# Optimization experiments

Hardware: AMD Instinct MI355X
Metric: run time of the kernel (lower is better)

Reference implementation:

```python
import jax, jax.numpy as jnp
import numpy as np

EMBED_DIM = 256
N_LEVELS = 4
N_HEADS = 8
N_POINTS = 4
HEAD_DIM = EMBED_DIM // N_HEADS
N_QUERIES = 8192
BATCH = 2
LEVEL_SHAPES = np.array([[128, 128], [64, 64], [32, 32], [16, 16]], dtype=np.int32)
HMAX, WMAX = 128, 128
EPS = 1e-5


def setup_inputs() -> dict:
    key = jax.random.key(0)
    ks = jax.random.split(key, 10)
    scale = 1.0 / np.sqrt(EMBED_DIM)
    query = jax.random.normal(ks[0], (N_QUERIES, EMBED_DIM), jnp.float32)
    xy_reference_points = jax.random.uniform(ks[1], (N_QUERIES, 2), jnp.float32, 0.05, 0.95)
    val = jax.random.normal(ks[2], (BATCH, HMAX, WMAX, N_LEVELS, EMBED_DIM), jnp.float32)
    # zero outside each level's valid support (mimics sparse COO: absent entries read as 0)
    hh = jnp.arange(HMAX)[:, None, None]
    ww = jnp.arange(WMAX)[None, :, None]
    lh = jnp.asarray(LEVEL_SHAPES[:, 0])[None, None, :]
    lw = jnp.asarray(LEVEL_SHAPES[:, 1])[None, None, :]
    mask = ((hh < lh) & (ww < lw)).astype(jnp.float32)
    stacked_value_tensors = val * mask[None, :, :, :, None]
    return {
        "query": query,
        "xy_reference_points": xy_reference_points,
        "stacked_value_tensors": stacked_value_tensors,
        "W_off": (jax.random.normal(ks[3], (EMBED_DIM, N_LEVELS * N_POINTS * N_HEADS * 2)) * scale * 0.1).astype(jnp.float32),
        "b_off": (jax.random.normal(ks[4], (N_LEVELS * N_POINTS * N_HEADS * 2,)) * 0.5).astype(jnp.float32),
        "W_attn": (jax.random.normal(ks[5], (EMBED_DIM, N_LEVELS * N_POINTS * N_HEADS)) * scale).astype(jnp.float32),
        "b_attn": jnp.zeros((N_LEVELS * N_POINTS * N_HEADS,), jnp.float32),
        "W_out": (jax.random.normal(ks[6], (EMBED_DIM, EMBED_DIM)) * scale).astype(jnp.float32),
        "b_out": jnp.zeros((EMBED_DIM,), jnp.float32),
        "batch_offsets": jnp.array([0, N_QUERIES // 2], jnp.int32),
        "spatial_shapes": jnp.asarray(LEVEL_SHAPES, jnp.int32),
    }


def reference(query, xy_reference_points, stacked_value_tensors, W_off, b_off,
              W_attn, b_attn, W_out, b_out, batch_offsets, spatial_shapes):
    Q = query.shape[0]
    # sampling offsets & attention weights (torch Linear with W stored [in,out])
    off = (query @ W_off + b_off).reshape(Q, N_LEVELS, N_POINTS, N_HEADS, 2)
    aw = (query @ W_attn + b_attn).reshape(Q, N_LEVELS * N_POINTS, N_HEADS)
    aw = jax.nn.softmax(aw, axis=1).reshape(Q, N_LEVELS, N_POINTS, N_HEADS)
    # sampling locations: sigmoid(inverse_sigmoid(ref) + offsets), then map (0,1)->(-1,1)
    r = jnp.clip(xy_reference_points, 0.0, 1.0)
    inv = jnp.log(jnp.clip(r, EPS, 1.0) / jnp.clip(1.0 - r, EPS, 1.0))
    loc = jax.nn.sigmoid(inv[:, None, None, None, :] + off) * 2.0 - 1.0  # (Q,L,P,H,2)
    # per-query batch index from batch_offsets (start index per batch element)
    bidx = jnp.searchsorted(batch_offsets, jnp.arange(Q), side="right") - 1  # (Q,)
    b = bidx[:, None, None, None]
    h_sz = spatial_shapes[:, 0].astype(loc.dtype)[None, :, None, None]
    w_sz = spatial_shapes[:, 1].astype(loc.dtype)[None, :, None, None]
    x = ((loc[..., 0] + 1.0) * w_sz - 1.0) / 2.0  # (Q,L,P,H)
    y = ((loc[..., 1] + 1.0) * h_sz - 1.0) / 2.0
    x0 = jnp.floor(x).astype(jnp.int32); x1 = x0 + 1
    y0 = jnp.floor(y).astype(jnp.int32); y1 = y0 + 1
    wcap = (spatial_shapes[:, 1] - 1).astype(jnp.int32)[None, :, None, None]
    hcap = (spatial_shapes[:, 0] - 1).astype(jnp.int32)[None, :, None, None]
    x0 = jnp.clip(x0, 0, wcap); x1 = jnp.clip(x1, 0, wcap)
    y0 = jnp.clip(y0, 0, hcap); y1 = jnp.clip(y1, 0, hcap)
    x0f = x0.astype(x.dtype); x1f = x1.astype(x.dtype)
    y0f = y0.astype(y.dtype); y1f = y1.astype(y.dtype)
    wa = (x1f - x) * (y1f - y)  # pairs with (x0,y0), as in source
    wb = (x1f - x) * (y - y0f)  # (x0,y1)
    wc = (x - x0f) * (y1f - y)  # (x1,y0)
    wd = (x - x0f) * (y - y0f)  # (x1,y1)
    V = stacked_value_tensors.reshape(BATCH, HMAX, WMAX, N_LEVELS, N_HEADS, HEAD_DIM)
    l = jnp.arange(N_LEVELS)[None, :, None, None]
    h = jnp.arange(N_HEADS)[None, None, None, :]
    # NOTE: source indexes (batch, x, y, level, head) -> x indexes the height dim; levels are square
    def g(xi, yi):
        return V[b, xi, yi, l, h]  # (Q,L,P,H,HEAD_DIM)
    sampled = (wa[..., None] * g(x0, y0) + wb[..., None] * g(x0, y1)
               + wc[..., None] * g(x1, y0) + wd[..., None] * g(x1, y1))
    out = jnp.einsum("qlphd,qlph->qhd", sampled, aw).reshape(Q, EMBED_DIM)
    return out @ W_out + b_out
```

## Files before the change

kernel.cpp:

```cpp
#include <hip/hip_runtime.h>
#include <math.h>

#define ED      256
#define NL      4
#define NH      8
#define NP      4
#define HD      32
#define HMAX    128
#define WMAX    128
#define NLP     16
#define NC      128
#define NOFF_AW 384
#define QPB     4
#define BSTRIDE (HMAX*WMAX*NL*ED)
#define XSTRIDE (WMAX*NL*ED)
#define YSTRIDE (NL*ED)

typedef __attribute__((ext_vector_type(8))) short bf16x8;
typedef __attribute__((ext_vector_type(4))) float f32x4;

__device__ __forceinline__ unsigned short f2bf(float x) {
    unsigned int u = __float_as_uint(x);
    u = (u + 0x7fffu + ((u >> 16) & 1u)) >> 16;
    return (unsigned short)u;
}
__device__ __forceinline__ float bf2f(unsigned short h) {
    unsigned int u = ((unsigned int)h) << 16;
    return __uint_as_float(u);
}

__global__ __launch_bounds__(256) void msda_convert_kernel(
    const float* __restrict__ query,
    const float* __restrict__ W_off,
    const float* __restrict__ W_attn,
    const float* __restrict__ W_out,
    unsigned short* __restrict__ qh,
    unsigned short* __restrict__ ql,
    unsigned short* __restrict__ BTh,
    unsigned short* __restrict__ BTl,
    unsigned short* __restrict__ WoutT,
    int nq)
{
    const int idx = blockIdx.x * 256 + threadIdx.x;
    const int t1 = nq * ED;
    const int t2 = NOFF_AW * ED;
    const int t3 = ED * ED;
    if (idx < t1) {
        float v = query[idx];
        unsigned short h = f2bf(v);
        qh[idx] = h;
        ql[idx] = f2bf(v - bf2f(h));
    } else if (idx < t1 + t2) {
        int i = idx - t1;
        int c = i >> 8, e = i & 255;
        float v = (c < ED) ? W_off[e * ED + c] : W_attn[e * NC + (c - ED)];
        unsigned short h = f2bf(v);
        BTh[i] = h;
        BTl[i] = f2bf(v - bf2f(h));
    } else if (idx < t1 + t2 + t3) {
        int i = idx - t1 - t2;
        int c = i >> 8, e = i & 255;
        WoutT[i] = f2bf(W_out[e * ED + c]);
    }
}

__global__ __launch_bounds__(256) void gemm_split_kernel(
    const unsigned short* __restrict__ Ah,
    const unsigned short* __restrict__ Al,
    const unsigned short* __restrict__ BTh,
    const unsigned short* __restrict__ BTl,
    const float* __restrict__ bias0,
    const float* __restrict__ bias1,
    float* __restrict__ C,
    int M, int NTOT, int bias_split)
{
    const int wave = threadIdx.x >> 6;
    const int lane = threadIdx.x & 63;
    const int gw   = blockIdx.x * 4 + wave;
    const int ngroups = NTOT >> 6;
    const int mg = gw / ngroups, ng = gw % ngroups;
    const int m16 = mg * 16, n64 = ng * 64;
    if (m16 >= M) return;

    const int mrow = lane & 15;
    const int quad = lane >> 4;

    const bf16x8* Ahp = (const bf16x8*)(Ah + (size_t)(m16 + mrow) * 256 + quad * 8);
    const bf16x8* Alp = (const bf16x8*)(Al + (size_t)(m16 + mrow) * 256 + quad * 8);
    const bf16x8* Bh0 = (const bf16x8*)(BTh + (size_t)(n64 +  0 + mrow) * 256 + quad * 8);
    const bf16x8* Bh1 = (const bf16x8*)(BTh + (size_t)(n64 + 16 + mrow) * 256 + quad * 8);
    const bf16x8* Bh2 = (const bf16x8*)(BTh + (size_t)(n64 + 32 + mrow) * 256 + quad * 8);
    const bf16x8* Bh3 = (const bf16x8*)(BTh + (size_t)(n64 + 48 + mrow) * 256 + quad * 8);
    const bf16x8* Bl0 = (const bf16x8*)(BTl + (size_t)(n64 +  0 + mrow) * 256 + quad * 8);
    const bf16x8* Bl1 = (const bf16x8*)(BTl + (size_t)(n64 + 16 + mrow) * 256 + quad * 8);
    const bf16x8* Bl2 = (const bf16x8*)(BTl + (size_t)(n64 + 32 + mrow) * 256 + quad * 8);
    const bf16x8* Bl3 = (const bf16x8*)(BTl + (size_t)(n64 + 48 + mrow) * 256 + quad * 8);

    f32x4 acc0 = {0.f,0.f,0.f,0.f}, acc1 = acc0, acc2 = acc0, acc3 = acc0;
    #pragma unroll
    for (int kb = 0; kb < 8; ++kb) {
        bf16x8 ah = Ahp[kb * 4];
        bf16x8 al = Alp[kb * 4];
        bf16x8 b0 = Bh0[kb * 4], b1 = Bh1[kb * 4], b2 = Bh2[kb * 4], b3 = Bh3[kb * 4];
        acc0 = __builtin_amdgcn_mfma_f32_16x16x32_bf16(ah, b0, acc0, 0, 0, 0);
        acc1 = __builtin_amdgcn_mfma_f32_16x16x32_bf16(ah, b1, acc1, 0, 0, 0);
        acc2 = __builtin_amdgcn_mfma_f32_16x16x32_bf16(ah, b2, acc2, 0, 0, 0);
        acc3 = __builtin_amdgcn_mfma_f32_16x16x32_bf16(ah, b3, acc3, 0, 0, 0);
        acc0 = __builtin_amdgcn_mfma_f32_16x16x32_bf16(al, b0, acc0, 0, 0, 0);
        acc1 = __builtin_amdgcn_mfma_f32_16x16x32_bf16(al, b1, acc1, 0, 0, 0);
        acc2 = __builtin_amdgcn_mfma_f32_16x16x32_bf16(al, b2, acc2, 0, 0, 0);
        acc3 = __builtin_amdgcn_mfma_f32_16x16x32_bf16(al, b3, acc3, 0, 0, 0);
        acc0 = __builtin_amdgcn_mfma_f32_16x16x32_bf16(ah, Bl0[kb * 4], acc0, 0, 0, 0);
        acc1 = __builtin_amdgcn_mfma_f32_16x16x32_bf16(ah, Bl1[kb * 4], acc1, 0, 0, 0);
        acc2 = __builtin_amdgcn_mfma_f32_16x16x32_bf16(ah, Bl2[kb * 4], acc2, 0, 0, 0);
        acc3 = __builtin_amdgcn_mfma_f32_16x16x32_bf16(ah, Bl3[kb * 4], acc3, 0, 0, 0);
    }

    const int col = lane & 15;
    f32x4 accs[4] = {acc0, acc1, acc2, acc3};
    #pragma unroll
    for (int i = 0; i < 4; ++i) {
        int n = n64 + i * 16 + col;
        float b = (n < bias_split) ? bias0[n] : bias1[n - bias_split];
        #pragma unroll
        for (int r = 0; r < 4; ++r) {
            int row = m16 + quad * 4 + r;
            C[(size_t)row * NTOT + n] = accs[i][r] + b;
        }
    }
}

__global__ __launch_bounds__(256) void gemm_bf16_kernel(
    const unsigned short* __restrict__ A,
    const unsigned short* __restrict__ BT,
    const float* __restrict__ bias,
    float* __restrict__ C,
    int M, int NTOT)
{
    const int wave = threadIdx.x >> 6;
    const int lane = threadIdx.x & 63;
    const int gw   = blockIdx.x * 4 + wave;
    const int ngroups = NTOT >> 6;
    const int mg = gw / ngroups, ng = gw % ngroups;
    const int m16 = mg * 16, n64 = ng * 64;
    if (m16 >= M) return;

    const int mrow = lane & 15;
    const int quad = lane >> 4;

    const bf16x8* Arow = (const bf16x8*)(A + (size_t)(m16 + mrow) * 256 + quad * 8);
    const bf16x8* B0 = (const bf16x8*)(BT + (size_t)(n64 +  0 + mrow) * 256 + quad * 8);
    const bf16x8* B1 = (const bf16x8*)(BT + (size_t)(n64 + 16 + mrow) * 256 + quad * 8);
    const bf16x8* B2 = (const bf16x8*)(BT + (size_t)(n64 + 32 + mrow) * 256 + quad * 8);
    const bf16x8* B3 = (const bf16x8*)(BT + (size_t)(n64 + 48 + mrow) * 256 + quad * 8);

    f32x4 acc0 = {0.f,0.f,0.f,0.f}, acc1 = acc0, acc2 = acc0, acc3 = acc0;
    #pragma unroll
    for (int kb = 0; kb < 8; ++kb) {
        bf16x8 af = Arow[kb * 4];
        acc0 = __builtin_amdgcn_mfma_f32_16x16x32_bf16(af, B0[kb * 4], acc0, 0, 0, 0);
        acc1 = __builtin_amdgcn_mfma_f32_16x16x32_bf16(af, B1[kb * 4], acc1, 0, 0, 0);
        acc2 = __builtin_amdgcn_mfma_f32_16x16x32_bf16(af, B2[kb * 4], acc2, 0, 0, 0);
        acc3 = __builtin_amdgcn_mfma_f32_16x16x32_bf16(af, B3[kb * 4], acc3, 0, 0, 0);
    }

    const int col = lane & 15;
    f32x4 accs[4] = {acc0, acc1, acc2, acc3};
    #pragma unroll
    for (int i = 0; i < 4; ++i) {
        int n = n64 + i * 16 + col;
        float b = bias[n];
        #pragma unroll
        for (int r = 0; r < 4; ++r) {
            int row = m16 + quad * 4 + r;
            C[(size_t)row * NTOT + n] = accs[i][r] + b;
        }
    }
}

__global__ __launch_bounds__(256) void msda_sample_kernel(
    const float* __restrict__ refp,
    const float* __restrict__ V,
    const float* __restrict__ off_aw,
    const int*   __restrict__ batch_off,
    int n_batch,
    const int*   __restrict__ spatial,
    unsigned short* __restrict__ out_pre,
    int q_total)
{
    __shared__ float  law[QPB][NC];
    __shared__ float2 sminv[QPB][NH];
    __shared__ float2 sref[QPB];
    __shared__ int4   soff[QPB][NC];
    __shared__ float4 swt[QPB][NC];

    const int t  = threadIdx.x;
    const int q0 = blockIdx.x * QPB;

    {
        const int s = t >> 6, c = t & 63;
        const float* row = off_aw + (size_t)(q0 + s) * NOFF_AW + ED;
        law[s][c]      = row[c];
        law[s][c + 64] = row[c + 64];
    }
    __syncthreads();

    if (t < QPB * NH) {
        const int s = t >> 3, h = t & 7;
        float m = -1e30f;
        #pragma unroll
        for (int lp = 0; lp < NLP; ++lp) m = fmaxf(m, law[s][lp * NH + h]);
        float sum = 0.f;
        #pragma unroll
        for (int lp = 0; lp < NLP; ++lp) sum += __expf(law[s][lp * NH + h] - m);
        sminv[s][h] = make_float2(m, 1.f / sum);
    } else if (t < QPB * NH + QPB) {
        const int s = t - QPB * NH;
        const int qid = q0 + s;
        float rx = refp[qid * 2 + 0], ry = refp[qid * 2 + 1];
        rx = fminf(fmaxf(rx, 0.f), 1.f);
        ry = fminf(fmaxf(ry, 0.f), 1.f);
        float ivx = __logf(fmaxf(rx, 1e-5f) / fmaxf(1.f - rx, 1e-5f));
        float ivy = __logf(fmaxf(ry, 1e-5f) / fmaxf(1.f - ry, 1e-5f));
        sref[s] = make_float2(ivx, ivy);
    }
    __syncthreads();

    {
        const int s = t >> 6;
        const int qid = q0 + s;
        int b = 0;
        for (int i = 1; i < n_batch; ++i)
            if (batch_off[i] <= qid) b = i;
        const int bbase = b * BSTRIDE;
        const float2 iv = sref[s];
        const float* offrow = off_aw + (size_t)qid * NOFF_AW;

        #pragma unroll
        for (int half = 0; half < 2; ++half) {
            const int c = (t & 63) + half * 64;
            const int l = c >> 5;
            const int h = c & 7;
            const int hsz = spatial[l * 2 + 0];
            const int wsz = spatial[l * 2 + 1];
            const int wcap = wsz - 1, hcap = hsz - 1;

            const float2 mi = sminv[s][h];
            const float a = __expf(law[s][c] - mi.x) * mi.y;

            const float ox = offrow[c * 2 + 0], oy = offrow[c * 2 + 1];
            float lx = 2.f / (1.f + __expf(-(iv.x + ox))) - 1.f;
            float ly = 2.f / (1.f + __expf(-(iv.y + oy))) - 1.f;
            float x = ((lx + 1.f) * (float)wsz - 1.f) * 0.5f;
            float y = ((ly + 1.f) * (float)hsz - 1.f) * 0.5f;
            int x0 = (int)floorf(x), y0 = (int)floorf(y);
            int x1 = x0 + 1, y1 = y0 + 1;
            x0 = min(max(x0, 0), wcap); x1 = min(max(x1, 0), wcap);
            y0 = min(max(y0, 0), hcap); y1 = min(max(y1, 0), hcap);
            float x0f = (float)x0, x1f = (float)x1;
            float y0f = (float)y0, y1f = (float)y1;

            float4 w;
            w.x = a * (x1f - x) * (y1f - y);
            w.y = a * (x1f - x) * (y - y0f);
            w.z = a * (x - x0f) * (y1f - y);
            w.w = a * (x - x0f) * (y - y0f);
            swt[s][c] = w;
            const int lbase = bbase + l * ED;
            int4 o;
            o.x = lbase + x0 * XSTRIDE + y0 * YSTRIDE;
            o.y = lbase + x0 * XSTRIDE + y1 * YSTRIDE;
            o.z = lbase + x1 * XSTRIDE + y0 * YSTRIDE;
            o.w = lbase + x1 * XSTRIDE + y1 * YSTRIDE;
            soff[s][c] = o;
        }
    }
    __syncthreads();

    {
        const int s    = t >> 6;
        const int lane = t & 63;
        const int h    = lane >> 3;
        const int d4   = (lane & 7) << 2;
        const int inner = h * HD + d4;
        float4 acc = {0.f, 0.f, 0.f, 0.f};
        #pragma unroll 4
        for (int lp = 0; lp < NLP; ++lp) {
            const int c = lp * NH + h;
            int4   o = soff[s][c];
            float4 w = swt[s][c];
            float4 v0 = *(const float4*)&V[o.x + inner];
            float4 v1 = *(const float4*)&V[o.y + inner];
            float4 v2 = *(const float4*)&V[o.z + inner];
            float4 v3 = *(const float4*)&V[o.w + inner];
            acc.x += w.x*v0.x + w.y*v1.x + w.z*v2.x + w.w*v3.x;
            acc.y += w.x*v0.y + w.y*v1.y + w.z*v2.y + w.w*v3.y;
            acc.z += w.x*v0.z + w.y*v1.z + w.z*v2.z + w.w*v3.z;
            acc.w += w.x*v0.w + w.y*v1.w + w.z*v2.w + w.w*v3.w;
        }
        ushort4 o4;
        o4.x = f2bf(acc.x); o4.y = f2bf(acc.y);
        o4.z = f2bf(acc.z); o4.w = f2bf(acc.w);
        *(ushort4*)&out_pre[(size_t)(q0 + s) * ED + inner] = o4;
    }
}

extern "C" void kernel_launch(void* const* d_in, const int* in_sizes, int n_in,
                              void* d_out, int out_size, void* d_ws, size_t ws_size,
                              hipStream_t stream) {
    const float* query  = (const float*)d_in[0];
    const float* refp   = (const float*)d_in[1];
    const float* V      = (const float*)d_in[2];
    const float* W_off  = (const float*)d_in[3];
    const float* b_off  = (const float*)d_in[4];
    const float* W_attn = (const float*)d_in[5];
    const float* b_attn = (const float*)d_in[6];
    const float* W_out  = (const float*)d_in[7];
    const float* b_out  = (const float*)d_in[8];
    const int*   boff   = (const int*)d_in[9];
    const int*   spat   = (const int*)d_in[10];
    const int n_batch   = in_sizes[9];
    const int nq        = in_sizes[0] / ED;
    float* out = (float*)d_out;

    char* ws = (char*)d_ws;
    float*          off_aw  = (float*)ws;
    unsigned short* qh      = (unsigned short*)(ws + (size_t)nq*NOFF_AW*4);
    unsigned short* ql      = qh    + (size_t)nq*ED;
    unsigned short* BTh     = ql    + (size_t)nq*ED;
    unsigned short* BTl     = BTh   + NOFF_AW*ED;
    unsigned short* WoutT   = BTl   + NOFF_AW*ED;
    unsigned short* out_pre = WoutT + ED*ED;

    {
        int total = nq*ED + NOFF_AW*ED + ED*ED;
        msda_convert_kernel<<<(total + 255)/256, 256, 0, stream>>>(
            query, W_off, W_attn, W_out, qh, ql, BTh, BTl, WoutT, nq);
    }
    {
        int waves = (nq/16) * (NOFF_AW/64);
        gemm_split_kernel<<<(waves + 3)/4, 256, 0, stream>>>(
            qh, ql, BTh, BTl, b_off, b_attn, off_aw, nq, NOFF_AW, ED);
    }
    {
        msda_sample_kernel<<<nq/QPB, 256, 0, stream>>>(
            refp, V, off_aw, boff, n_batch, spat, out_pre, nq);
    }
    {
        int waves = (nq/16) * (ED/64);
        gemm_bf16_kernel<<<(waves + 3)/4, 256, 0, stream>>>(
            out_pre, WoutT, b_out, out, nq, ED);
    }
}
```

Before: 290.1 us.

## Switch offset GEMM to fp16 split-A with in-kernel query conversion

Replaces the bf16 hi/lo three-term split GEMM with an fp16 scheme: the weights are stored as a single fp16 copy and the fp32 query is split into fp16 hi/lo inside the GEMM kernel, so only two MFMA passes run per k-step. This removes the separate query conversion pass and its workspace writes and reads, and cuts MFMA count by a third. fp16's longer mantissa is meant to keep offset precision without the weight-low term, but it risks range and rounding differences in the computed offsets.

```diff
diff --git a/kernel.cpp b/kernel.cpp
--- a/kernel.cpp
+++ b/kernel.cpp
@@ -16,59 +16,40 @@
 #define XSTRIDE (WMAX*NL*ED)
 #define YSTRIDE (NL*ED)
 
-typedef __attribute__((ext_vector_type(8))) short bf16x8;
-typedef __attribute__((ext_vector_type(4))) float f32x4;
+typedef __attribute__((ext_vector_type(8))) short    bf16x8;
+typedef __attribute__((ext_vector_type(8))) __fp16   f16x8;
+typedef __attribute__((ext_vector_type(4))) float    f32x4;
 
 __device__ __forceinline__ unsigned short f2bf(float x) {
     unsigned int u = __float_as_uint(x);
     u = (u + 0x7fffu + ((u >> 16) & 1u)) >> 16;
     return (unsigned short)u;
 }
-__device__ __forceinline__ float bf2f(unsigned short h) {
-    unsigned int u = ((unsigned int)h) << 16;
-    return __uint_as_float(u);
-}
-
-__global__ __launch_bounds__(256) void msda_convert_kernel(
-    const float* __restrict__ query,
+
+__global__ __launch_bounds__(256) void msda_wconv_kernel(
     const float* __restrict__ W_off,
     const float* __restrict__ W_attn,
     const float* __restrict__ W_out,
-    unsigned short* __restrict__ qh,
-    unsigned short* __restrict__ ql,
-    unsigned short* __restrict__ BTh,
-    unsigned short* __restrict__ BTl,
-    unsigned short* __restrict__ WoutT,
-    int nq)
+    __fp16*         __restrict__ WcatT,
+    unsigned short* __restrict__ WoutT)
 {
     const int idx = blockIdx.x * 256 + threadIdx.x;
-    const int t1 = nq * ED;
     const int t2 = NOFF_AW * ED;
     const int t3 = ED * ED;
-    if (idx < t1) {
-        float v = query[idx];
-        unsigned short h = f2bf(v);
-        qh[idx] = h;
-        ql[idx] = f2bf(v - bf2f(h));
-    } else if (idx < t1 + t2) {
-        int i = idx - t1;
-        int c = i >> 8, e = i & 255;
+    if (idx < t2) {
+        int c = idx >> 8, e = idx & 255;
         float v = (c < ED) ? W_off[e * ED + c] : W_attn[e * NC + (c - ED)];
-        unsigned short h = f2bf(v);
-        BTh[i] = h;
-        BTl[i] = f2bf(v - bf2f(h));
-    } else if (idx < t1 + t2 + t3) {
-        int i = idx - t1 - t2;
+        WcatT[idx] = (__fp16)v;
+    } else if (idx < t2 + t3) {
+        int i = idx - t2;
         int c = i >> 8, e = i & 255;
         WoutT[i] = f2bf(W_out[e * ED + c]);
     }
 }
 
-__global__ __launch_bounds__(256) void gemm_split_kernel(
-    const unsigned short* __restrict__ Ah,
-    const unsigned short* __restrict__ Al,
-    const unsigned short* __restrict__ BTh,
-    const unsigned short* __restrict__ BTl,
+__global__ __launch_bounds__(256) void gemm_f16_kernel(
+    const float*  __restrict__ A,
+    const __fp16* __restrict__ BT,
     const float* __restrict__ bias0,
     const float* __restrict__ bias1,
     float* __restrict__ C,
@@ -85,35 +66,34 @@
     const int mrow = lane & 15;
     const int quad = lane >> 4;
 
-    const bf16x8* Ahp = (const bf16x8*)(Ah + (size_t)(m16 + mrow) * 256 + quad * 8);
-    const bf16x8* Alp = (const bf16x8*)(Al + (size_t)(m16 + mrow) * 256 + quad * 8);
-    const bf16x8* Bh0 = (const bf16x8*)(BTh + (size_t)(n64 +  0 + mrow) * 256 + quad * 8);
-    const bf16x8* Bh1 = (const bf16x8*)(BTh + (size_t)(n64 + 16 + mrow) * 256 + quad * 8);
-    const bf16x8* Bh2 = (const bf16x8*)(BTh + (size_t)(n64 + 32 + mrow) * 256 + quad * 8);
-    const bf16x8* Bh3 = (const bf16x8*)(BTh + (size_t)(n64 + 48 + mrow) * 256 + quad * 8);
-    const bf16x8* Bl0 = (const bf16x8*)(BTl + (size_t)(n64 +  0 + mrow) * 256 + quad * 8);
-    const bf16x8* Bl1 = (const bf16x8*)(BTl + (size_t)(n64 + 16 + mrow) * 256 + quad * 8);
-    const bf16x8* Bl2 = (const bf16x8*)(BTl + (size_t)(n64 + 32 + mrow) * 256 + quad * 8);
-    const bf16x8* Bl3 = (const bf16x8*)(BTl + (size_t)(n64 + 48 + mrow) * 256 + quad * 8);
+    const float4* Arow = (const float4*)(A + (size_t)(m16 + mrow) * 256 + quad * 8);
+    const f16x8* B0 = (const f16x8*)(BT + (size_t)(n64 +  0 + mrow) * 256 + quad * 8);
+    const f16x8* B1 = (const f16x8*)(BT + (size_t)(n64 + 16 + mrow) * 256 + quad * 8);
+    const f16x8* B2 = (const f16x8*)(BT + (size_t)(n64 + 32 + mrow) * 256 + quad * 8);
+    const f16x8* B3 = (const f16x8*)(BT + (size_t)(n64 + 48 + mrow) * 256 + quad * 8);
 
     f32x4 acc0 = {0.f,0.f,0.f,0.f}, acc1 = acc0, acc2 = acc0, acc3 = acc0;
     #pragma unroll
     for (int kb = 0; kb < 8; ++kb) {
-        bf16x8 ah = Ahp[kb * 4];
-        bf16x8 al = Alp[kb * 4];
-        bf16x8 b0 = Bh0[kb * 4], b1 = Bh1[kb * 4], b2 = Bh2[kb * 4], b3 = Bh3[kb * 4];
-        acc0 = __builtin_amdgcn_mfma_f32_16x16x32_bf16(ah, b0, acc0, 0, 0, 0);
-        acc1 = __builtin_amdgcn_mfma_f32_16x16x32_bf16(ah, b1, acc1, 0, 0, 0);
-        acc2 = __builtin_amdgcn_mfma_f32_16x16x32_bf16(ah, b2, acc2, 0, 0, 0);
-        acc3 = __builtin_amdgcn_mfma_f32_16x16x32_bf16(ah, b3, acc3, 0, 0, 0);
-        acc0 = __builtin_amdgcn_mfma_f32_16x16x32_bf16(al, b0, acc0, 0, 0, 0);
-        acc1 = __builtin_amdgcn_mfma_f32_16x16x32_bf16(al, b1, acc1, 0, 0, 0);
-        acc2 = __builtin_amdgcn_mfma_f32_16x16x32_bf16(al, b2, acc2, 0, 0, 0);
-        acc3 = __builtin_amdgcn_mfma_f32_16x16x32_bf16(al, b3, acc3, 0, 0, 0);
-        acc0 = __builtin_amdgcn_mfma_f32_16x16x32_bf16(ah, Bl0[kb * 4], acc0, 0, 0, 0);
-        acc1 = __builtin_amdgcn_mfma_f32_16x16x32_bf16(ah, Bl1[kb * 4], acc1, 0, 0, 0);
-        acc2 = __builtin_amdgcn_mfma_f32_16x16x32_bf16(ah, Bl2[kb * 4], acc2, 0, 0, 0);
-        acc3 = __builtin_amdgcn_mfma_f32_16x16x32_bf16(ah, Bl3[kb * 4], acc3, 0, 0, 0);
+        float4 a0 = Arow[kb * 8 + 0];
+        float4 a1 = Arow[kb * 8 + 1];
+        float av[8] = {a0.x, a0.y, a0.z, a0.w, a1.x, a1.y, a1.z, a1.w};
+        f16x8 ah, al;
+        #pragma unroll
+        for (int j = 0; j < 8; ++j) {
+            __fp16 h = (__fp16)av[j];
+            ah[j] = h;
+            al[j] = (__fp16)(av[j] - (float)h);
+        }
+        f16x8 b0 = B0[kb * 4], b1 = B1[kb * 4], b2 = B2[kb * 4], b3 = B3[kb * 4];
+        acc0 = __builtin_amdgcn_mfma_f32_16x16x32_f16(ah, b0, acc0, 0, 0, 0);
+        acc1 = __builtin_amdgcn_mfma_f32_16x16x32_f16(ah, b1, acc1, 0, 0, 0);
+        acc2 = __builtin_amdgcn_mfma_f32_16x16x32_f16(ah, b2, acc2, 0, 0, 0);
+        acc3 = __builtin_amdgcn_mfma_f32_16x16x32_f16(ah, b3, acc3, 0, 0, 0);
+        acc0 = __builtin_amdgcn_mfma_f32_16x16x32_f16(al, b0, acc0, 0, 0, 0);
+        acc1 = __builtin_amdgcn_mfma_f32_16x16x32_f16(al, b1, acc1, 0, 0, 0);
+        acc2 = __builtin_amdgcn_mfma_f32_16x16x32_f16(al, b2, acc2, 0, 0, 0);
+        acc3 = __builtin_amdgcn_mfma_f32_16x16x32_f16(al, b3, acc3, 0, 0, 0);
     }
 
     const int col = lane & 15;
@@ -325,22 +305,19 @@
 
     char* ws = (char*)d_ws;
     float*          off_aw  = (float*)ws;
-    unsigned short* qh      = (unsigned short*)(ws + (size_t)nq*NOFF_AW*4);
-    unsigned short* ql      = qh    + (size_t)nq*ED;
-    unsigned short* BTh     = ql    + (size_t)nq*ED;
-    unsigned short* BTl     = BTh   + NOFF_AW*ED;
-    unsigned short* WoutT   = BTl   + NOFF_AW*ED;
+    __fp16*         WcatT   = (__fp16*)(ws + (size_t)nq*NOFF_AW*4);
+    unsigned short* WoutT   = (unsigned short*)(WcatT + NOFF_AW*ED);
     unsigned short* out_pre = WoutT + ED*ED;
 
     {
-        int total = nq*ED + NOFF_AW*ED + ED*ED;
-        msda_convert_kernel<<<(total + 255)/256, 256, 0, stream>>>(
-            query, W_off, W_attn, W_out, qh, ql, BTh, BTl, WoutT, nq);
+        int total = NOFF_AW*ED + ED*ED;
+        msda_wconv_kernel<<<(total + 255)/256, 256, 0, stream>>>(
+            W_off, W_attn, W_out, WcatT, WoutT);
     }
     {
         int waves = (nq/16) * (NOFF_AW/64);
-        gemm_split_kernel<<<(waves + 3)/4, 256, 0, stream>>>(
-            qh, ql, BTh, BTl, b_off, b_attn, off_aw, nq, NOFF_AW, ED);
+        gemm_f16_kernel<<<(waves + 3)/4, 256, 0, stream>>>(
+            query, WcatT, b_off, b_attn, off_aw, nq, NOFF_AW, ED);
     }
     {
         msda_sample_kernel<<<nq/QPB, 256, 0, stream>>>(
```

Result: faster. 274.8 us (-5.3%).
